# Performance work log

Hardware: AMD Instinct MI355X
Metric: run time of the kernel (lower is better)

## Reference

```python
import jax, jax.numpy as jnp
import numpy as np

B, R, S, T, F = 16, 4, 4, 14, 2048  # batch, rx ants, streams, ofdm symbols, subcarriers


def setup_inputs() -> dict:
    key = jax.random.key(0)
    ks = jax.random.split(key, 5)
    y_re = jax.random.normal(ks[0], (B, R, T, F), jnp.float32)
    y_im = jax.random.normal(ks[1], (B, R, T, F), jnp.float32)
    h_re = jax.random.normal(ks[2], (B, R, S, T, F), jnp.float32)
    h_im = jax.random.normal(ks[3], (B, R, S, T, F), jnp.float32)
    mask = jax.random.randint(ks[4], (T, F), 0, 2, jnp.int32)  # MU_MIMO_RG_populated
    noise_var = jnp.array([0.1], jnp.float32)
    return {"y_re": y_re, "y_im": y_im, "h_re": h_re, "h_im": h_im,
            "mask": mask, "noise_var": noise_var}


def _sic_lmmse(y, h, no):
    # y: [B,T,F,R] complex, h: [B,T,F,R,S] complex, no: scalar noise variance
    eyeS = jnp.eye(S, dtype=jnp.complex64)
    y_res = y
    xs, ns = [], []
    for k in range(S):  # fixed detection order over the 4 streams
        m = (jnp.arange(S) >= k).astype(jnp.complex64)  # remaining (undetected) streams
        Hm = h * m  # zero out already-cancelled stream columns
        gram0 = jnp.einsum('...rs,...rt->...st', jnp.conj(Hm), Hm)  # [.,S,S] Hm^H Hm
        A = gram0 + no * eyeS                                        # LMMSE matrix
        Ainv = jnp.linalg.inv(A)                                     # batched 4x4 inverse
        z = jnp.einsum('...rs,...r->...s', jnp.conj(Hm), y_res)     # Hm^H y_res
        xz = jnp.einsum('...st,...t->...s', Ainv, z)                 # unbiased-unscaled estimate
        d = jnp.einsum('...t,...t->...', Ainv[..., k, :], gram0[..., :, k])  # (Ainv gram0)_kk
        xk = xz[..., k] / d                                          # bias-corrected LMMSE estimate
        ne = jnp.real((1.0 - d) / d)                                 # effective post-eq noise var
        y_res = y_res - h[..., :, k] * xk[..., None]                 # soft interference cancellation
        xs.append(xk)
        ns.append(ne)
    x_hat = jnp.stack(xs, -1)   # [B,T,F,S]
    no_eff = jnp.stack(ns, -1)  # [B,T,F,S]
    return x_hat, no_eff


def reference(y_re, y_im, h_re, h_im, mask, noise_var):
    y = jax.lax.complex(y_re, y_im)             # [B,R,T,F]
    h = jax.lax.complex(h_re, h_im)             # [B,R,S,T,F]
    y = jnp.transpose(y, (0, 2, 3, 1))          # [B,T,F,R]
    h = jnp.transpose(h, (0, 3, 4, 1, 2))       # [B,T,F,R,S]
    no = noise_var[0]
    x_hat, no_eff = _sic_lmmse(y, h, no)
    m = mask.astype(jnp.float32)[None, :, :, None]  # populated-RE mask [1,T,F,1]
    x_hat = x_hat * m
    no_eff = no_eff * m
    x_hat = jnp.transpose(x_hat, (0, 3, 1, 2))   # [B,S,T,F]
    no_eff = jnp.transpose(no_eff, (0, 3, 1, 2))
    x_ri = jnp.stack([jnp.real(x_hat), jnp.imag(x_hat)], 0)  # [2,B,S,T,F] real view
    return x_ri, no_eff
```

## Files before the change

kernel.cpp:

```cpp
#include <hip/hip_runtime.h>

#define B_ 16
#define R_ 4
#define S_ 4
#define T_ 14
#define F_ 2048
constexpr int P_ = F_ / 2;

typedef float vf __attribute__((ext_vector_type(2)));

struct cplx { vf re, im; };

__device__ __forceinline__ vf vsp(float s){ vf r; r.x = s; r.y = s; return r; }
__device__ __forceinline__ vf vrcp(vf x){ vf r; r.x = __builtin_amdgcn_rcpf(x.x); r.y = __builtin_amdgcn_rcpf(x.y); return r; }
__device__ __forceinline__ vf vrsq(vf x){ vf r; r.x = __builtin_amdgcn_rsqf(x.x); r.y = __builtin_amdgcn_rsqf(x.y); return r; }

__device__ __forceinline__ cplx cmul(cplx a, cplx b) {
    return {a.re*b.re - a.im*b.im, a.re*b.im + a.im*b.re};
}
__device__ __forceinline__ cplx cmulc(cplx a, cplx b) {
    return {a.re*b.re + a.im*b.im, a.re*b.im - a.im*b.re};
}
__device__ __forceinline__ cplx cadd(cplx a, cplx b){ return {a.re+b.re, a.im+b.im}; }
__device__ __forceinline__ cplx csub(cplx a, cplx b){ return {a.re-b.re, a.im-b.im}; }
__device__ __forceinline__ cplx cscale(cplx a, vf s){ return {a.re*s, a.im*s}; }
__device__ __forceinline__ cplx conjc(cplx a){ return {a.re, -a.im}; }

__global__ __launch_bounds__(256) void sic_lmmse_kernel(
    const float* __restrict__ y_re_, const float* __restrict__ y_im_,
    const float* __restrict__ h_re_, const float* __restrict__ h_im_,
    const int* __restrict__ mask, const float* __restrict__ nv,
    float* __restrict__ out_)
{
    constexpr int N    = B_ * T_ * P_;
    constexpr int BSTP = B_ * S_ * T_ * P_;

    int idx = blockIdx.x * 256 + threadIdx.x;
    int fv = idx % P_;
    int bt = idx / P_;
    int t  = bt % T_;
    int b  = bt / T_;

    const vf* y_re = (const vf*)y_re_;
    const vf* y_im = (const vf*)y_im_;
    const vf* h_re = (const vf*)h_re_;
    const vf* h_im = (const vf*)h_im_;
    vf*       out  = (vf*)out_;

    float no  = nv[0];
    vf    vno = vsp(no);

    int2 mi = ((const int2*)mask)[t * P_ + fv];
    vf m; m.x = (float)mi.x; m.y = (float)mi.y;

    cplx g[4][4];
    cplx z[4];
    #pragma unroll
    for (int i = 0; i < 4; i++) {
        z[i] = { vsp(0.f), vsp(0.f) };
        #pragma unroll
        for (int j = 0; j <= i; j++) g[i][j] = { vsp(0.f), vsp(0.f) };
    }

    #pragma unroll
    for (int r = 0; r < 4; r++) {
        int ybase = ((b * R_ + r) * T_ + t) * P_ + fv;
        cplx yr = { y_re[ybase], y_im[ybase] };
        cplx hr[4];
        #pragma unroll
        for (int s = 0; s < 4; s++) {
            int hbase = (((b * R_ + r) * S_ + s) * T_ + t) * P_ + fv;
            hr[s] = { h_re[hbase], h_im[hbase] };
        }
        #pragma unroll
        for (int s = 0; s < 4; s++) {
            z[s] = cadd(z[s], cmulc(hr[s], yr));
            #pragma unroll
            for (int u = 0; u <= s; u++)
                g[s][u] = cadd(g[s][u], cmulc(hr[s], hr[u]));
        }
    }

    cplx Lm[4][4];
    vf dinv[4];
    #pragma unroll
    for (int i = 0; i < 4; i++) {
        #pragma unroll
        for (int j = 0; j < i; j++) {
            cplx s = g[i][j];
            #pragma unroll
            for (int p = 0; p < j; p++)
                s = csub(s, cmul(Lm[i][p], conjc(Lm[j][p])));
            Lm[i][j] = cscale(s, dinv[j]);
        }
        vf dd = g[i][i].re + vno;
        #pragma unroll
        for (int p = 0; p < i; p++)
            dd = dd - (Lm[i][p].re * Lm[i][p].re + Lm[i][p].im * Lm[i][p].im);
        dinv[i] = vrsq(dd);
    }

    cplx M[4][4];
    #pragma unroll
    for (int i = 0; i < 4; i++) {
        #pragma unroll
        for (int j = 0; j < i; j++) {
            cplx s = { vsp(0.f), vsp(0.f) };
            #pragma unroll
            for (int p = j; p < i; p++)
                s = cadd(s, cmul(Lm[i][p], M[p][j]));
            M[i][j] = cscale(s, -dinv[i]);
        }
        M[i][i] = { dinv[i], vsp(0.f) };
    }

    cplx W[4][4];
    #pragma unroll
    for (int i = 0; i < 4; i++) {
        #pragma unroll
        for (int j = 0; j <= i; j++) {
            cplx s = { vsp(0.f), vsp(0.f) };
            #pragma unroll
            for (int p = i; p < 4; p++)
                s = cadd(s, cmul(conjc(M[p][i]), M[p][j]));
            W[i][j] = s;
        }
    }

    cplx zc[4];
    #pragma unroll
    for (int j = 0; j < 4; j++) zc[j] = z[j];

    #pragma unroll
    for (int k = 0; k < 4; k++) {
        const int n = 4 - k;
        vf e = W[0][0].re;
        cplx xz = cscale(zc[0], e);
        #pragma unroll
        for (int j = 1; j < 4; j++) {
            if (j < n) xz = cadd(xz, cmul(conjc(W[j][0]), zc[j]));
        }
        vf d    = vsp(1.0f) - vno * e;
        vf drcp = vrcp(d);
        cplx xk = cscale(xz, drcp);
        vf ne   = vno * e * drcp;

        int obase = ((b * S_ + k) * T_ + t) * P_ + fv;
        out[obase]            = xk.re * m;
        out[BSTP + obase]     = xk.im * m;
        out[2 * BSTP + obase] = ne * m;

        if (k < 3) {
            vf einv = vrcp(e);
            #pragma unroll
            for (int j = 1; j < 4; j++) {
                if (j < n) zc[j - 1] = csub(zc[j], cmul(g[k + j][k], xk));
            }
            cplx W2[3][3];
            #pragma unroll
            for (int i = 1; i < 4; i++) {
                #pragma unroll
                for (int j = 1; j <= i; j++) {
                    if (i < n)
                        W2[i - 1][j - 1] =
                            csub(W[i][j], cscale(cmul(W[i][0], conjc(W[j][0])), einv));
                }
            }
            #pragma unroll
            for (int i = 0; i < 3; i++) {
                #pragma unroll
                for (int j = 0; j <= i; j++) {
                    if (i < n - 1) W[i][j] = W2[i][j];
                }
            }
        }
    }
}

extern "C" void kernel_launch(void* const* d_in, const int* in_sizes, int n_in,
                              void* d_out, int out_size, void* d_ws, size_t ws_size,
                              hipStream_t stream) {
    const float* y_re = (const float*)d_in[0];
    const float* y_im = (const float*)d_in[1];
    const float* h_re = (const float*)d_in[2];
    const float* h_im = (const float*)d_in[3];
    const int*   mask = (const int*)  d_in[4];
    const float* nv   = (const float*)d_in[5];
    float* out = (float*)d_out;

    constexpr int N = B_ * T_ * P_;
    int threads = 256;
    int blocks  = N / threads;
    hipLaunchKernelGGL(sic_lmmse_kernel, dim3(blocks), dim3(threads), 0, stream,
                       y_re, y_im, h_re, h_im, mask, nv, out);
}
```

Measured before the change: 113.0 us.

## Replace explicit inverse and downdates with reverse-order Cholesky and triangular solves

Uses an upper-triangular factorization built from the last stream backward, so that each SIC step's bias term comes straight from the diagonal (dinv[k]^2) and the estimate from a back-substitution on the residual matched filter. This removes the explicit triangular inverse, the W = M^H M product and the per-step Schur-complement downdates of W. It adds a triangular solve per step and slightly changes the floating-point path of the result. The Gram diagonal is now accumulated as real norms only.

```diff
diff --git a/kernel.cpp b/kernel.cpp
--- a/kernel.cpp
+++ b/kernel.cpp
@@ -25,6 +25,7 @@
 __device__ __forceinline__ cplx csub(cplx a, cplx b){ return {a.re-b.re, a.im-b.im}; }
 __device__ __forceinline__ cplx cscale(cplx a, vf s){ return {a.re*s, a.im*s}; }
 __device__ __forceinline__ cplx conjc(cplx a){ return {a.re, -a.im}; }
+__device__ __forceinline__ vf cnorm(cplx a){ return a.re*a.re + a.im*a.im; }
 
 __global__ __launch_bounds__(256) void sic_lmmse_kernel(
     const float* __restrict__ y_re_, const float* __restrict__ y_im_,
@@ -32,7 +33,6 @@
     const int* __restrict__ mask, const float* __restrict__ nv,
     float* __restrict__ out_)
 {
-    constexpr int N    = B_ * T_ * P_;
     constexpr int BSTP = B_ * S_ * T_ * P_;
 
     int idx = blockIdx.x * 256 + threadIdx.x;
@@ -53,13 +53,15 @@
     int2 mi = ((const int2*)mask)[t * P_ + fv];
     vf m; m.x = (float)mi.x; m.y = (float)mi.y;
 
-    cplx g[4][4];
+    cplx go[4][4];
+    vf   gd[4];
     cplx z[4];
     #pragma unroll
     for (int i = 0; i < 4; i++) {
-        z[i] = { vsp(0.f), vsp(0.f) };
+        z[i]  = { vsp(0.f), vsp(0.f) };
+        gd[i] = vsp(0.f);
         #pragma unroll
-        for (int j = 0; j <= i; j++) g[i][j] = { vsp(0.f), vsp(0.f) };
+        for (int j = 0; j < i; j++) go[i][j] = { vsp(0.f), vsp(0.f) };
     }
 
     #pragma unroll
@@ -74,56 +76,29 @@
         }
         #pragma unroll
         for (int s = 0; s < 4; s++) {
-            z[s] = cadd(z[s], cmulc(hr[s], yr));
+            z[s]  = cadd(z[s], cmulc(hr[s], yr));
+            gd[s] = gd[s] + hr[s].re * hr[s].re + hr[s].im * hr[s].im;
             #pragma unroll
-            for (int u = 0; u <= s; u++)
-                g[s][u] = cadd(g[s][u], cmulc(hr[s], hr[u]));
+            for (int u = 0; u < s; u++)
+                go[s][u] = cadd(go[s][u], cmulc(hr[s], hr[u]));
         }
     }
 
-    cplx Lm[4][4];
+    cplx U[4][4];
     vf dinv[4];
     #pragma unroll
-    for (int i = 0; i < 4; i++) {
+    for (int i = 3; i >= 0; i--) {
+        vf dd = gd[i] + vno;
         #pragma unroll
-        for (int j = 0; j < i; j++) {
-            cplx s = g[i][j];
+        for (int p = i + 1; p < 4; p++) dd = dd - cnorm(U[i][p]);
+        dinv[i] = vrsq(dd);
+        #pragma unroll
+        for (int j = i - 1; j >= 0; j--) {
+            cplx s = conjc(go[i][j]);
             #pragma unroll
-            for (int p = 0; p < j; p++)
-                s = csub(s, cmul(Lm[i][p], conjc(Lm[j][p])));
-            Lm[i][j] = cscale(s, dinv[j]);
-        }
-        vf dd = g[i][i].re + vno;
-        #pragma unroll
-        for (int p = 0; p < i; p++)
-            dd = dd - (Lm[i][p].re * Lm[i][p].re + Lm[i][p].im * Lm[i][p].im);
-        dinv[i] = vrsq(dd);
-    }
-
-    cplx M[4][4];
-    #pragma unroll
-    for (int i = 0; i < 4; i++) {
-        #pragma unroll
-        for (int j = 0; j < i; j++) {
-            cplx s = { vsp(0.f), vsp(0.f) };
-            #pragma unroll
-            for (int p = j; p < i; p++)
-                s = cadd(s, cmul(Lm[i][p], M[p][j]));
-            M[i][j] = cscale(s, -dinv[i]);
-        }
-        M[i][i] = { dinv[i], vsp(0.f) };
-    }
-
-    cplx W[4][4];
-    #pragma unroll
-    for (int i = 0; i < 4; i++) {
-        #pragma unroll
-        for (int j = 0; j <= i; j++) {
-            cplx s = { vsp(0.f), vsp(0.f) };
-            #pragma unroll
-            for (int p = i; p < 4; p++)
-                s = cadd(s, cmul(conjc(M[p][i]), M[p][j]));
-            W[i][j] = s;
+            for (int p = i + 1; p < 4; p++)
+                s = csub(s, cmul(U[j][p], conjc(U[i][p])));
+            U[j][i] = cscale(s, dinv[i]);
         }
     }
 
@@ -133,16 +108,20 @@
 
     #pragma unroll
     for (int k = 0; k < 4; k++) {
-        const int n = 4 - k;
-        vf e = W[0][0].re;
-        cplx xz = cscale(zc[0], e);
+        cplx w[4];
         #pragma unroll
-        for (int j = 1; j < 4; j++) {
-            if (j < n) xz = cadd(xz, cmul(conjc(W[j][0]), zc[j]));
+        for (int i = 3; i >= k; i--) {
+            cplx s = zc[i];
+            #pragma unroll
+            for (int p = i + 1; p < 4; p++)
+                s = csub(s, cmul(U[i][p], w[p]));
+            w[i] = cscale(s, dinv[i]);
         }
+
+        vf e    = dinv[k] * dinv[k];
         vf d    = vsp(1.0f) - vno * e;
         vf drcp = vrcp(d);
-        cplx xk = cscale(xz, drcp);
+        cplx xk = cscale(w[k], dinv[k] * drcp);
         vf ne   = vno * e * drcp;
 
         int obase = ((b * S_ + k) * T_ + t) * P_ + fv;
@@ -151,28 +130,9 @@
         out[2 * BSTP + obase] = ne * m;
 
         if (k < 3) {
-            vf einv = vrcp(e);
             #pragma unroll
-            for (int j = 1; j < 4; j++) {
-                if (j < n) zc[j - 1] = csub(zc[j], cmul(g[k + j][k], xk));
-            }
-            cplx W2[3][3];
-            #pragma unroll
-            for (int i = 1; i < 4; i++) {
-                #pragma unroll
-                for (int j = 1; j <= i; j++) {
-                    if (i < n)
-                        W2[i - 1][j - 1] =
-                            csub(W[i][j], cscale(cmul(W[i][0], conjc(W[j][0])), einv));
-                }
-            }
-            #pragma unroll
-            for (int i = 0; i < 3; i++) {
-                #pragma unroll
-                for (int j = 0; j <= i; j++) {
-                    if (i < n - 1) W[i][j] = W2[i][j];
-                }
-            }
+            for (int j = k + 1; j < 4; j++)
+                zc[j] = csub(zc[j], cmul(go[j][k], xk));
         }
     }
 }
```

Result: no change. 112.3 us (-0.7%).
